# Kernel optimization log

Hardware: AMD Instinct MI355X
Metric: run time of the kernel (lower is better)

## Reference

```python
import jax, jax.numpy as jnp
import numpy as np

NUM_SPHERICAL = 7   # L
NUM_RADIAL = 6      # K
CUTOFF = 5.0
ENV_P = 6           # envelope exponent 5 -> p = exponent + 1
N_EDGES = 500000
N_PAIRS = 2000000


def _sph_jn_np(r, l):
    # spherical Bessel j_l via upward recurrence (numpy float64, host-side)
    j = np.sin(r) / r
    if l == 0:
        return j
    jp = np.sin(r) / r**2 - np.cos(r) / r
    for i in range(1, l):
        j, jp = jp, (2 * i + 1) / r * jp - j
    return jp


def _bessel_zeros(L, K):
    # zeros of j_0 are n*pi; zeros of j_l interlace zeros of j_{l-1} (bisection)
    prev = np.arange(1, K + L + 1, dtype=np.float64) * np.pi
    zeros = [prev[:K].copy()]
    for l in range(1, L):
        lo, hi = prev[:-1].copy(), prev[1:].copy()
        flo = _sph_jn_np(lo, l)
        for _ in range(100):
            mid = 0.5 * (lo + hi)
            fm = _sph_jn_np(mid, l)
            same = np.sign(fm) == np.sign(flo)
            lo = np.where(same, mid, lo)
            flo = np.where(same, fm, flo)
            hi = np.where(same, hi, mid)
        prev = 0.5 * (lo + hi)
        zeros.append(prev[:K].copy())
    return np.stack(zeros)  # (L, K)


_Z = _bessel_zeros(NUM_SPHERICAL, NUM_RADIAL)
_NORM = np.stack([1.0 / np.sqrt(0.5 * _sph_jn_np(_Z[l], l + 1) ** 2)
                  for l in range(NUM_SPHERICAL)])
Z = jnp.asarray(_Z, dtype=jnp.float32)        # (L, K) Bessel zeros z_{l,n}
NORM = jnp.asarray(_NORM, dtype=jnp.float32)  # (L, K) normalizers c_{l,n}
_SPH_C = jnp.asarray(np.sqrt((2 * np.arange(NUM_SPHERICAL) + 1) / (4 * np.pi)),
                     dtype=jnp.float32)       # Y_l^0 prefactors


def _sph_jn(t, l):
    # spherical Bessel j_l(t), upward recurrence (matches closed-form sympy basis)
    j = jnp.sin(t) / t
    if l == 0:
        return j
    jp = jnp.sin(t) / t**2 - jnp.cos(t) / t
    for i in range(1, l):
        j, jp = jp, (2 * i + 1) / t * jp - j
    return jp


def _envelope(x):
    # DimeNet polynomial envelope u(x) = 1/x + a x^{p-1} + b x^p + c x^{p+1}
    p = ENV_P
    a = -(p + 1) * (p + 2) / 2.0
    b = float(p * (p + 2))
    c = -p * (p + 1) / 2.0
    return 1.0 / x + a * x ** (p - 1) + b * x ** p + c * x ** (p + 1)


def setup_inputs() -> dict:
    key = jax.random.key(0)
    k1, k2, k3 = jax.random.split(key, 3)
    distances = jax.random.normal(k1, (N_EDGES, 3), dtype=jnp.float32) * 2.0
    senders = jax.random.randint(k2, (N_PAIRS,), 0, N_EDGES)
    receivers = jax.random.randint(k3, (N_PAIRS,), 0, N_EDGES)
    return {"distances": distances, "senders": senders, "receivers": receivers}


def reference(distances, senders, receivers):
    L, K = NUM_SPHERICAL, NUM_RADIAL
    dist = jnp.linalg.norm(distances, axis=-1, keepdims=True)     # (E, 1)
    normed_d = distances / dist                                   # (E, 3)
    x = dist / CUTOFF                                             # (E, 1)
    # radial Bessel basis: rbf[e, l, n] = c_{l,n} * j_l(z_{l,n} * x_e)
    rbf = jnp.stack([NORM[l] * _sph_jn(x * Z[l], l) for l in range(L)], axis=1)
    env = _envelope(x)                                            # (E, 1)
    rbf = rbf.reshape(-1, L * K) * env                            # (E, L*K)
    # angular basis: Y_l^0(theta) = sqrt((2l+1)/4pi) * P_l(cos theta)
    cos = jnp.einsum('pd,pd->p', normed_d[receivers], normed_d[senders])  # (P,)
    P_prev = jnp.ones_like(cos)
    P_cur = cos
    legs = [P_prev, P_cur]
    for l in range(1, L - 1):
        P_prev, P_cur = P_cur, ((2 * l + 1) * cos * P_cur - l * P_prev) / (l + 1)
        legs.append(P_cur)
    cbf = jnp.stack(legs[:L], axis=1) * _SPH_C                    # (P, L)
    # outer-product fuse: (P, L, K) -> (P, L*K)
    out = (rbf[senders].reshape(-1, L, K) * cbf[:, :, None]).reshape(-1, L * K)
    return out
```

## Files before the change

kernel.cpp:

```cpp
#include <hip/hip_runtime.h>
#include <math.h>

#define L_SPH 7
#define K_RAD 6
#define LK    42
#define TPB   256
#define PTPB  64
#define RSTR  48


typedef float f32x4 __attribute__((ext_vector_type(4)));
typedef float f32x2 __attribute__((ext_vector_type(2)));


struct SBConsts {
    float z[L_SPH][K_RAD];
    float nrm[L_SPH][K_RAD];
    float sphc[L_SPH];
};

static double host_sph_jn(double r, int l) {
    double j = sin(r) / r;
    if (l == 0) return j;
    double jp = sin(r) / (r * r) - cos(r) / r;
    for (int i = 1; i < l; i++) {
        double t = (2.0 * i + 1.0) / r * jp - j;
        j = jp; jp = t;
    }
    return jp;
}

static SBConsts make_consts() {
    const int L = L_SPH, K = K_RAD;
    double prev[L + K];
    for (int i = 0; i < L + K; i++) prev[i] = (i + 1) * M_PI;
    int plen = L + K;
    double zeros[L_SPH][K_RAD];
    for (int n = 0; n < K; n++) zeros[0][n] = prev[n];
    for (int l = 1; l < L; l++) {
        int m = plen - 1;
        double lo[L + K], hi[L + K], flo[L + K];
        for (int i = 0; i < m; i++) {
            lo[i] = prev[i]; hi[i] = prev[i + 1];
            flo[i] = host_sph_jn(lo[i], l);
        }
        for (int it = 0; it < 100; it++) {
            for (int i = 0; i < m; i++) {
                double mid = 0.5 * (lo[i] + hi[i]);
                double fm  = host_sph_jn(mid, l);
                bool same  = (fm >= 0.0) == (flo[i] >= 0.0);
                if (same) { lo[i] = mid; flo[i] = fm; }
                else      { hi[i] = mid; }
            }
        }
        for (int i = 0; i < m; i++) prev[i] = 0.5 * (lo[i] + hi[i]);
        plen = m;
        for (int n = 0; n < K; n++) zeros[l][n] = prev[n];
    }
    SBConsts c;
    for (int l = 0; l < L; l++) {
        for (int n = 0; n < K; n++) {
            c.z[l][n] = (float)zeros[l][n];
            double j1 = host_sph_jn(zeros[l][n], l + 1);
            c.nrm[l][n] = (float)(1.0 / sqrt(0.5 * j1 * j1));
        }
        c.sphc[l] = (float)sqrt((2.0 * l + 1.0) / (4.0 * M_PI));
    }
    return c;
}

__device__ __forceinline__ float sin_f32cr(float t) { return (float)sin((double)t); }
__device__ __forceinline__ void sincos_f32cr(float t, float& s, float& c) {
    double ds, dc;
    sincos((double)t, &ds, &dc);
    s = (float)ds; c = (float)dc;
}

__device__ __forceinline__ void legendre_cbf(float cs, const float* sphc,
                                             float* cbf) {
#pragma clang fp contract(off)
    float P0 = 1.0f, P1 = cs;
    cbf[0] = sphc[0];
    cbf[1] = sphc[1] * cs;
#pragma unroll
    for (int l = 1; l < L_SPH - 1; l++) {
        float a  = (float)(2 * l + 1) * cs;
        float b  = a * P1;
        float d  = b - (float)l * P0;
        float Pn = d / (float)(l + 1);
        P0 = P1; P1 = Pn;
        cbf[l + 1] = sphc[l + 1] * Pn;
    }
}


__global__ __launch_bounds__(64) void init_tab(float* __restrict__ tab, SBConsts c) {
    if (blockIdx.x != 0 || threadIdx.x != 0) return;
#pragma unroll
    for (int l = 0; l < L_SPH; l++)
#pragma unroll
        for (int n = 0; n < K_RAD; n++) {
            tab[l * K_RAD + n]      = c.z[l][n];
            tab[42 + l * K_RAD + n] = c.nrm[l][n];
        }
}


__global__ __launch_bounds__(TPB) void edge_pre(
        const float* __restrict__ d, float* __restrict__ rbf,
        float4* __restrict__ nd4, int nE) {
#pragma clang fp contract(off)
    int e = blockIdx.x * TPB + threadIdx.x;
    if (e >= nE) return;
    float dx = d[3 * e], dy = d[3 * e + 1], dz = d[3 * e + 2];
    float s = dx * dx;
    s = s + dy * dy;
    s = s + dz * dz;
    float dist = (float)sqrt((double)s);
    float nx = dx / dist, ny = dy / dist, nz = dz / dist;
    float x = dist / 5.0f;
    float x2 = x * x, x4 = x2 * x2;
    float x5 = x4 * x, x6 = x5 * x, x7 = x6 * x;
    float env = 1.0f / x;
    env = env + (-28.0f) * x5;
    env = env + 48.0f * x6;
    env = env + (-21.0f) * x7;
    nd4[e] = make_float4(nx, ny, nz, 0.0f);
    float* row = rbf + (size_t)e * RSTR;
    f32x2 xe; xe.x = x; xe.y = env;
    *(f32x2*)(row + 42) = xe;
    f32x4 dir; dir.x = nx; dir.y = ny; dir.z = nz; dir.w = 0.0f;
    *(f32x4*)(row + 44) = dir;
}


__global__ __launch_bounds__(TPB, 4) void edge_basis(
        const float* __restrict__ tab, float* __restrict__ rbf, int nE) {
#pragma clang fp contract(off)
    int i = blockIdx.x * TPB + threadIdx.x;
    if (i >= nE * LK) return;
    unsigned ui = (unsigned)i;
    unsigned e = ui / (unsigned)LK;
    int j = (int)(ui - e * (unsigned)LK);
    const float* row = rbf + (size_t)e * RSTR;
    f32x2 xe = *(const f32x2*)(row + 42);
    float x = xe.x, env = xe.y;
    float zj = tab[j], nrmj = tab[42 + j];
    int l = j / K_RAD;
    float t = x * zj;
    float sn, co;
    if (l == 0) { sn = sin_f32cr(t); co = 0.0f; }
    else        { sincos_f32cr(t, sn, co); }
    float jj = sn / t;
    if (l > 0) {
        float t2 = t * t;
        float a1 = sn / t2;
        float a2 = co / t;
        float jp = a1 - a2;
        for (int ii = 1; ii < l; ii++) {
            float q  = (float)(2 * ii + 1) / t;
            float m  = q * jp;
            float nj = m - jj;
            jj = jp; jp = nj;
        }
        jj = jp;
    }
    float rb = nrmj * jj;
    rbf[(size_t)e * RSTR + j] = rb * env;
}


__global__ __launch_bounds__(PTPB, 4) void pair_kernel(
        const int* __restrict__ snd, const int* __restrict__ rcv,
        const float* __restrict__ rbf, const float4* __restrict__ nd4,
        float* __restrict__ out, int nP, SBConsts c) {
#pragma clang fp contract(off)
    __shared__ float so[PTPB * LK];
    int p = blockIdx.x * PTPB + threadIdx.x;
    if (p < nP) {
        int s = snd[p], r = rcv[p];
        const float4* rowp = (const float4*)(rbf + (size_t)s * RSTR);
        float4 v[12];
#pragma unroll
        for (int q = 0; q < 12; q++) v[q] = rowp[q];
        float4 b = nd4[r];
        float ax = v[11].x, ay = v[11].y, az = v[11].z;
        float cs = ax * b.x;
        cs = cs + ay * b.y;
        cs = cs + az * b.z;
        float cbf[L_SPH];
        legendre_cbf(cs, c.sphc, cbf);
        float2* my = (float2*)&so[threadIdx.x * LK];
#pragma unroll
        for (int q = 0; q < 10; q++) {
            float4 vq = v[q];
            my[2 * q]     = make_float2(vq.x * cbf[(4 * q + 0) / K_RAD],
                                        vq.y * cbf[(4 * q + 1) / K_RAD]);
            my[2 * q + 1] = make_float2(vq.z * cbf[(4 * q + 2) / K_RAD],
                                        vq.w * cbf[(4 * q + 3) / K_RAD]);
        }
        my[20] = make_float2(v[10].x * cbf[6], v[10].y * cbf[6]);
    }
    __syncthreads();
    size_t base  = (size_t)blockIdx.x * (PTPB * LK);
    size_t limit = (size_t)nP * LK;
    if (base + PTPB * LK <= limit) {
        f32x4* o4 = (f32x4*)(out + base);
        const f32x4* s4 = (const f32x4*)so;
#pragma unroll
        for (int k = 0; k < 10; k++)
            __builtin_nontemporal_store(s4[threadIdx.x + k * PTPB],
                                        &o4[threadIdx.x + k * PTPB]);
        f32x2* o2 = (f32x2*)(out + base + 2560);
        const f32x2* s2 = (const f32x2*)(so + 2560);
        __builtin_nontemporal_store(s2[threadIdx.x], &o2[threadIdx.x]);
    } else {
        for (int k = 0; k < LK; k++) {
            size_t g = base + threadIdx.x + (size_t)k * PTPB;
            if (g < limit) out[g] = so[threadIdx.x + k * PTPB];
        }
    }
}


__device__ void edge_row_f32(float dx, float dy, float dz, const SBConsts& c,
                             float* row, float& nx, float& ny, float& nz) {
#pragma clang fp contract(off)
    float s = dx * dx;
    s = s + dy * dy;
    s = s + dz * dz;
    float dist = (float)sqrt((double)s);
    nx = dx / dist; ny = dy / dist; nz = dz / dist;
    float x = dist / 5.0f;
    float x2 = x * x, x4 = x2 * x2;
    float x5 = x4 * x, x6 = x5 * x, x7 = x6 * x;
    float env = 1.0f / x;
    env = env + (-28.0f) * x5;
    env = env + 48.0f * x6;
    env = env + (-21.0f) * x7;
#pragma unroll
    for (int l = 0; l < L_SPH; l++) {
#pragma unroll
        for (int n = 0; n < K_RAD; n++) {
            float t  = x * c.z[l][n];
            float sn, co;
            if (l == 0) { sn = sin_f32cr(t); co = 0.0f; }
            else        { sincos_f32cr(t, sn, co); }
            float j  = sn / t;
            if (l > 0) {
                float t2 = t * t;
                float a1 = sn / t2;
                float a2 = co / t;
                float jp = a1 - a2;
#pragma unroll
                for (int i = 1; i < l; i++) {
                    float q  = (float)(2 * i + 1) / t;
                    float m  = q * jp;
                    float nj = m - j;
                    j = jp; jp = nj;
                }
                j = jp;
            }
            float rb = c.nrm[l][n] * j;
            row[l * K_RAD + n] = rb * env;
        }
    }
}

__global__ __launch_bounds__(TPB) void fused_kernel(
        const float* __restrict__ d, const int* __restrict__ snd,
        const int* __restrict__ rcv, float* __restrict__ out,
        int nP, SBConsts c) {
#pragma clang fp contract(off)
    int p = blockIdx.x * TPB + threadIdx.x;
    if (p >= nP) return;
    int s = snd[p], r = rcv[p];
    float row[LK], sx, sy, sz;
    edge_row_f32(d[3 * s], d[3 * s + 1], d[3 * s + 2], c, row, sx, sy, sz);
    float rx = d[3 * r], ry = d[3 * r + 1], rz = d[3 * r + 2];
    float t = rx * rx;  t = t + ry * ry;  t = t + rz * rz;
    float rd = (float)sqrt((double)t);
    float cs = sx * (rx / rd);
    cs = cs + sy * (ry / rd);
    cs = cs + sz * (rz / rd);
    float cbf[L_SPH];
    legendre_cbf(cs, c.sphc, cbf);
    float* o = out + (size_t)p * LK;
#pragma unroll
    for (int j = 0; j < LK; j++) o[j] = row[j] * cbf[j / K_RAD];
}


extern "C" void kernel_launch(void* const* d_in, const int* in_sizes, int n_in,
                              void* d_out, int out_size, void* d_ws, size_t ws_size,
                              hipStream_t stream) {
    static SBConsts c = make_consts();
    const float* dists = (const float*)d_in[0];
    const int*   snd   = (const int*)d_in[1];
    const int*   rcv   = (const int*)d_in[2];
    float*       out   = (float*)d_out;
    int nE = in_sizes[0] / 3;
    int nP = in_sizes[1];

    size_t rbf_b = (size_t)nE * RSTR * sizeof(float);
    size_t nd4_b = (size_t)nE * sizeof(float4);
    size_t tab_b = 512;
    size_t need  = rbf_b + nd4_b + tab_b;

    if (ws_size >= need) {
        float*  rbf = (float*)d_ws;
        float4* nd4 = (float4*)((char*)d_ws + rbf_b);
        float*  tab = (float*)((char*)d_ws + rbf_b + nd4_b);
        int nB = nE * LK;
        init_tab  <<<1, 64, 0, stream>>>(tab, c);
        edge_pre  <<<(nE + TPB - 1) / TPB, TPB, 0, stream>>>(dists, rbf, nd4, nE);
        edge_basis<<<(nB + TPB - 1) / TPB, TPB, 0, stream>>>(tab, rbf, nE);
        pair_kernel<<<(nP + PTPB - 1) / PTPB, PTPB, 0, stream>>>(snd, rcv, rbf, nd4, out, nP, c);
    } else {
        fused_kernel<<<(nP + TPB - 1) / TPB, TPB, 0, stream>>>(dists, snd, rcv, out, nP, c);
    }
}
```

Baseline: 591.0 us.

## Fuse edge precompute and Bessel basis kernels with LDS-staged coalesced row writes

Merges edge_pre and edge_basis into one kernel. Each block handles 64 edges: it computes distance, envelope and direction once per edge, then four waves evaluate the 42 basis terms into an LDS tile. The tile is written out as coalesced nontemporal 16-byte stores. This removes a launch and the global round-trip of x/env between kernels, at the cost of LDS use and less parallelism per basis element. Nontemporal stores may hurt L2 reuse when pair_kernel reads rbf right afterwards.

```diff
diff --git a/kernel.cpp b/kernel.cpp
--- a/kernel.cpp
+++ b/kernel.cpp
@@ -7,6 +7,8 @@
 #define TPB   256
 #define PTPB  64
 #define RSTR  48
+#define EPB   64
+#define LSTR  49
 
 
 typedef float f32x4 __attribute__((ext_vector_type(4)));
@@ -106,67 +108,84 @@
 }
 
 
-__global__ __launch_bounds__(TPB) void edge_pre(
-        const float* __restrict__ d, float* __restrict__ rbf,
-        float4* __restrict__ nd4, int nE) {
-#pragma clang fp contract(off)
-    int e = blockIdx.x * TPB + threadIdx.x;
-    if (e >= nE) return;
-    float dx = d[3 * e], dy = d[3 * e + 1], dz = d[3 * e + 2];
-    float s = dx * dx;
-    s = s + dy * dy;
-    s = s + dz * dz;
-    float dist = (float)sqrt((double)s);
-    float nx = dx / dist, ny = dy / dist, nz = dz / dist;
-    float x = dist / 5.0f;
-    float x2 = x * x, x4 = x2 * x2;
-    float x5 = x4 * x, x6 = x5 * x, x7 = x6 * x;
-    float env = 1.0f / x;
-    env = env + (-28.0f) * x5;
-    env = env + 48.0f * x6;
-    env = env + (-21.0f) * x7;
-    nd4[e] = make_float4(nx, ny, nz, 0.0f);
-    float* row = rbf + (size_t)e * RSTR;
-    f32x2 xe; xe.x = x; xe.y = env;
-    *(f32x2*)(row + 42) = xe;
-    f32x4 dir; dir.x = nx; dir.y = ny; dir.z = nz; dir.w = 0.0f;
-    *(f32x4*)(row + 44) = dir;
-}
-
-
-__global__ __launch_bounds__(TPB, 4) void edge_basis(
-        const float* __restrict__ tab, float* __restrict__ rbf, int nE) {
-#pragma clang fp contract(off)
-    int i = blockIdx.x * TPB + threadIdx.x;
-    if (i >= nE * LK) return;
-    unsigned ui = (unsigned)i;
-    unsigned e = ui / (unsigned)LK;
-    int j = (int)(ui - e * (unsigned)LK);
-    const float* row = rbf + (size_t)e * RSTR;
-    f32x2 xe = *(const f32x2*)(row + 42);
-    float x = xe.x, env = xe.y;
-    float zj = tab[j], nrmj = tab[42 + j];
-    int l = j / K_RAD;
-    float t = x * zj;
-    float sn, co;
-    if (l == 0) { sn = sin_f32cr(t); co = 0.0f; }
-    else        { sincos_f32cr(t, sn, co); }
-    float jj = sn / t;
-    if (l > 0) {
-        float t2 = t * t;
-        float a1 = sn / t2;
-        float a2 = co / t;
-        float jp = a1 - a2;
-        for (int ii = 1; ii < l; ii++) {
-            float q  = (float)(2 * ii + 1) / t;
-            float m  = q * jp;
-            float nj = m - jj;
-            jj = jp; jp = nj;
-        }
-        jj = jp;
-    }
-    float rb = nrmj * jj;
-    rbf[(size_t)e * RSTR + j] = rb * env;
+__global__ __launch_bounds__(TPB, 4) void edge_fused(
+        const float* __restrict__ d, const float* __restrict__ tab,
+        float* __restrict__ rbf, float4* __restrict__ nd4, int nE) {
+#pragma clang fp contract(off)
+    __shared__ float lds[EPB * LSTR];
+    __shared__ float xe[EPB * 2];
+    int t  = threadIdx.x;
+    int e0 = blockIdx.x * EPB;
+    int rows = nE - e0; if (rows > EPB) rows = EPB;
+
+    if (t < EPB && t < rows) {
+        int e = e0 + t;
+        float dx = d[3 * e], dy = d[3 * e + 1], dz = d[3 * e + 2];
+        float s = dx * dx;
+        s = s + dy * dy;
+        s = s + dz * dz;
+        float dist = (float)sqrt((double)s);
+        float nx = dx / dist, ny = dy / dist, nz = dz / dist;
+        float x = dist / 5.0f;
+        float x2 = x * x, x4 = x2 * x2;
+        float x5 = x4 * x, x6 = x5 * x, x7 = x6 * x;
+        float env = 1.0f / x;
+        env = env + (-28.0f) * x5;
+        env = env + 48.0f * x6;
+        env = env + (-21.0f) * x7;
+        nd4[e] = make_float4(nx, ny, nz, 0.0f);
+        xe[2 * t] = x; xe[2 * t + 1] = env;
+        float* lrow = &lds[t * LSTR];
+        lrow[42] = x;  lrow[43] = env;
+        lrow[44] = nx; lrow[45] = ny; lrow[46] = nz; lrow[47] = 0.0f;
+    }
+    __syncthreads();
+
+    int lane = t & 63, wid = t >> 6;
+    float x = xe[2 * lane], env = xe[2 * lane + 1];
+#pragma unroll 1
+    for (int cc = 0; cc < 11; cc++) {
+        int j = cc * 4 + wid;
+        if (j < LK && lane < rows) {
+            float zj = tab[j], nrmj = tab[42 + j];
+            int l = j / K_RAD;
+            float tt = x * zj;
+            float sn, co;
+            if (l == 0) { sn = sin_f32cr(tt); }
+            else        { sincos_f32cr(tt, sn, co); }
+            float jj = sn / tt;
+            if (l > 0) {
+                float t2 = tt * tt;
+                float a1 = sn / t2;
+                float a2 = co / tt;
+                float jp = a1 - a2;
+                for (int ii = 1; ii < l; ii++) {
+                    float q  = (float)(2 * ii + 1) / tt;
+                    float m  = q * jp;
+                    float nj = m - jj;
+                    jj = jp; jp = nj;
+                }
+                jj = jp;
+            }
+            float rb = nrmj * jj;
+            lds[lane * LSTR + j] = rb * env;
+        }
+    }
+    __syncthreads();
+
+    float* obase = rbf + (size_t)e0 * RSTR;
+    int nvec = rows * (RSTR / 4);
+#pragma unroll
+    for (int k = 0; k < 3; k++) {
+        int idx4 = t + k * TPB;
+        if (idx4 < nvec) {
+            int r  = idx4 / 12;
+            int c4 = idx4 - r * 12;
+            const float* lp = &lds[r * LSTR + c4 * 4];
+            f32x4 v; v.x = lp[0]; v.y = lp[1]; v.z = lp[2]; v.w = lp[3];
+            __builtin_nontemporal_store(v, (f32x4*)obase + idx4);
+        }
+    }
 }
 
 
@@ -311,10 +330,8 @@
         float*  rbf = (float*)d_ws;
         float4* nd4 = (float4*)((char*)d_ws + rbf_b);
         float*  tab = (float*)((char*)d_ws + rbf_b + nd4_b);
-        int nB = nE * LK;
         init_tab  <<<1, 64, 0, stream>>>(tab, c);
-        edge_pre  <<<(nE + TPB - 1) / TPB, TPB, 0, stream>>>(dists, rbf, nd4, nE);
-        edge_basis<<<(nB + TPB - 1) / TPB, TPB, 0, stream>>>(tab, rbf, nE);
+        edge_fused<<<(nE + EPB - 1) / EPB, TPB, 0, stream>>>(dists, tab, rbf, nd4, nE);
         pair_kernel<<<(nP + PTPB - 1) / PTPB, PTPB, 0, stream>>>(snd, rcv, rbf, nd4, out, nP, c);
     } else {
         fused_kernel<<<(nP + TPB - 1) / TPB, TPB, 0, stream>>>(dists, snd, rcv, out, nP, c);
```

Result: faster. 537.9 us (-9.0%).
